# Performance work log

Measured on AMD Instinct MI355X. Metric: run time of the kernel, lower is better.

## Reference

```python
import jax, jax.numpy as jnp
import numpy as np

N_USERS = 50000
N_ENT = 100000
N_EDGES = 2_000_000
N_INTER = 1_000_000
CHANNEL = 64
N_HEADS = 2
D_K = CHANNEL // N_HEADS
N_HOPS = 2
N_REL = 10  # relation_emb has N_REL-1 rows


def setup_inputs() -> dict:
    key = jax.random.key(0)
    ks = jax.random.split(key, 8)
    user_emb = jax.random.normal(ks[0], (N_USERS, CHANNEL), jnp.float32) * 0.1
    entity_emb = jax.random.normal(ks[1], (N_ENT, CHANNEL), jnp.float32) * 0.1
    relation_emb = jax.random.normal(ks[2], (N_REL - 1, CHANNEL), jnp.float32) * 0.1
    W_Q = jax.random.normal(ks[3], (CHANNEL, CHANNEL), jnp.float32) * (1.0 / np.sqrt(CHANNEL))
    edge_index = jax.random.randint(ks[4], (2, N_EDGES), 0, N_ENT)
    edge_type = jax.random.randint(ks[5], (N_EDGES,), 1, N_REL)  # in [1, N_REL-1]
    inter_edge = jnp.stack([
        jax.random.randint(ks[6], (N_INTER,), 0, N_USERS),
        jax.random.randint(ks[7], (N_INTER,), 0, N_ENT),
    ])
    inter_edge_w = jnp.full((N_INTER,), 1.0 / 20.0, jnp.float32)
    return {
        "user_emb": user_emb,
        "entity_emb": entity_emb,
        "relation_emb": relation_emb,
        "W_Q": W_Q,
        "inter_edge_w": inter_edge_w,
        "edge_index": edge_index,
        "edge_type": edge_type,
        "inter_edge": inter_edge,
    }


def _l2norm(x):
    # F.normalize(dim=-1) with eps=1e-12
    n = jnp.linalg.norm(x, axis=-1, keepdims=True)
    return x / jnp.maximum(n, 1e-12)


def _scatter_softmax(logits, seg, num_segments):
    # per-segment (over leading axis) numerically-stable softmax; logits [E, H]
    m = jax.ops.segment_max(logits, seg, num_segments=num_segments)
    e = jnp.exp(logits - m[seg])
    s = jax.ops.segment_sum(e, seg, num_segments=num_segments)
    return e / s[seg]


def reference(user_emb, entity_emb, relation_emb, W_Q, inter_edge_w,
              edge_index, edge_type, inter_edge):
    head, tail = edge_index[0], edge_index[1]
    u_idx, i_idx = inter_edge[0], inter_edge[1]
    rel = relation_emb[edge_type - 1]  # [E, C]
    inv_sqrt_dk = 1.0 / np.sqrt(D_K)

    entity_res, user_res = entity_emb, user_emb
    for _ in range(N_HOPS):
        h_emb = entity_emb[head]                       # [E, C]
        t_emb = entity_emb[tail]                       # [E, C]
        q = (h_emb @ W_Q).reshape(-1, N_HEADS, D_K)    # [E, H, Dk]
        k = (t_emb @ W_Q).reshape(-1, N_HEADS, D_K) * rel.reshape(-1, N_HEADS, D_K)
        score = (q * k).sum(-1) * inv_sqrt_dk          # [E, H]
        attn = _scatter_softmax(score, head, N_ENT)    # [E, H]
        value = (t_emb * rel).reshape(-1, N_HEADS, D_K)
        agg = (value * attn[..., None]).reshape(-1, CHANNEL)
        entity_agg = jax.ops.segment_sum(agg, head, num_segments=N_ENT)
        item_agg = inter_edge_w[:, None] * entity_emb[i_idx]
        user_agg = jax.ops.segment_sum(item_agg, u_idx, num_segments=N_USERS)
        # mess_dropout disabled (eval mode)
        entity_emb = _l2norm(entity_agg)
        user_emb = _l2norm(user_agg)
        entity_res = entity_res + entity_emb
        user_res = user_res + user_emb
    return entity_res, user_res
```

## Files before the change

### kernel.cpp

```cpp
#include <hip/hip_runtime.h>

#define NU     50000
#define NEN    100000
#define NEDGE  2000000
#define NINTER 1000000
#define CH     64
#define NRELM1 9
#define CAPE   64
#define CAPU   64

#define BINSH   8
#define NBINE   ((NEN + 255) >> BINSH)
#define NBINU   ((NU  + 255) >> BINSH)
#define CHUNKE  8192
#define CHUNKU  4096
#define NBE_BLK ((NEDGE  + CHUNKE - 1) / CHUNKE)
#define NBU_BLK ((NINTER + CHUNKU - 1) / CHUNKU)
#define DSTRE   416
#define DSTRU   224
#define NSTR_E  ((NEN * CH) / 2048)
#define NSTR_U  ((NU * CH + 2047) / 2048)

typedef _Float16 hv2 __attribute__((ext_vector_type(2)));
typedef _Float16 h8  __attribute__((ext_vector_type(8)));
typedef float    f32x4 __attribute__((ext_vector_type(4)));
union P4 { float4 f; hv2 h[4]; };

static __device__ __forceinline__ hv2 pkrtz(float a, float b) {
    return __builtin_bit_cast(hv2, __builtin_amdgcn_cvt_pkrtz(a, b));
}


__global__ __launch_bounds__(256) void k_bin(
    const float* __restrict__ ue, const float* __restrict__ ee,
    const float* __restrict__ re, const float* __restrict__ wq,
    const float* __restrict__ iw, const int* __restrict__ eidx,
    const int* __restrict__ etype, const int* __restrict__ ii,
    _Float16* __restrict__ QE, float* __restrict__ Eres, float* __restrict__ Ures,
    _Float16* __restrict__ Relh, _Float16* __restrict__ Wt,
    unsigned* __restrict__ dirE, unsigned* __restrict__ dirU,
    int* __restrict__ blkBufE, unsigned long long* __restrict__ blkBufU)
{
    __shared__ long long srt64[CHUNKU];
    __shared__ int hist[512];
    __shared__ int sc[512];
    int* srt = (int*)srt64;
    int b = blockIdx.x, tid = threadIdx.x;

    if (b < NBE_BLK) {
        hist[tid] = 0; hist[tid + 256] = 0;
        __syncthreads();
        int base = b * CHUNKE;
        int n = NEDGE - base; if (n > CHUNKE) n = CHUNKE;
        for (int i = tid; i < n; i += 256)
            atomicAdd(&hist[eidx[base + i] >> BINSH], 1);
        __syncthreads();
        sc[tid] = hist[tid]; sc[tid + 256] = hist[tid + 256];
        __syncthreads();
#pragma unroll
        for (int off = 1; off < 512; off <<= 1) {
            int v0 = (tid >= off) ? sc[tid - off] : 0;
            int v1 = sc[tid + 256 - off];
            __syncthreads();
            sc[tid] += v0; sc[tid + 256] += v1;
            __syncthreads();
        }
        sc[tid] -= hist[tid]; sc[tid + 256] -= hist[tid + 256];
        __syncthreads();
        for (int i = tid; i < n; i += 256) {
            int h  = eidx[base + i];
            int t  = eidx[NEDGE + base + i];
            int rt = etype[base + i] - 1;
            int pos = atomicAdd(&sc[h >> BINSH], 1);
            srt[pos] = (h & 255) | ((t | (rt << 17)) << 8);
        }
        __syncthreads();
        int4* dst = (int4*)(blkBufE + b * CHUNKE);
        const int4* s4 = (const int4*)srt;
        for (int j = tid; j < ((n + 3) >> 2); j += 256) dst[j] = s4[j];
        for (int bin = tid; bin < NBINE; bin += 256)
            dirE[b * DSTRE + bin] =
                ((unsigned)(sc[bin] - hist[bin]) << 16) | (unsigned)hist[bin];
    } else if (b < NBE_BLK + NBU_BLK) {
        hist[tid] = 0; hist[tid + 256] = 0;
        __syncthreads();
        int ub = b - NBE_BLK;
        int base = ub * CHUNKU;
        int n = NINTER - base; if (n > CHUNKU) n = CHUNKU;
        for (int i = tid; i < n; i += 256)
            atomicAdd(&hist[ii[base + i] >> BINSH], 1);
        __syncthreads();
        sc[tid] = hist[tid]; sc[tid + 256] = hist[tid + 256];
        __syncthreads();
#pragma unroll
        for (int off = 1; off < 512; off <<= 1) {
            int v0 = (tid >= off) ? sc[tid - off] : 0;
            int v1 = sc[tid + 256 - off];
            __syncthreads();
            sc[tid] += v0; sc[tid + 256] += v1;
            __syncthreads();
        }
        sc[tid] -= hist[tid]; sc[tid + 256] -= hist[tid + 256];
        __syncthreads();
        for (int i = tid; i < n; i += 256) {
            int u = ii[base + i];
            int e = ii[NINTER + base + i];
            unsigned w = __float_as_uint(iw[base + i]);
            int pos = atomicAdd(&sc[u >> BINSH], 1);
            srt64[pos] = (unsigned long long)((u & 255) | (e << 8))
                       | ((unsigned long long)w << 32);
        }
        __syncthreads();
        int4* dst = (int4*)(blkBufU + (size_t)ub * CHUNKU);
        const int4* s4 = (const int4*)srt64;
        for (int j = tid; j < ((n + 1) >> 1); j += 256) dst[j] = s4[j];
        for (int bin = tid; bin < NBINU; bin += 256)
            dirU[ub * DSTRU + bin] =
                ((unsigned)(sc[bin] - hist[bin]) << 16) | (unsigned)hist[bin];
    } else {
        int sb = b - (NBE_BLK + NBU_BLK);
        if (sb < NSTR_E) {
            int i0 = sb * 2048 + tid * 8;
            float4 a = *(const float4*)(ee + i0);
            float4 c = *(const float4*)(ee + i0 + 4);
            *(float4*)(Eres + i0)     = a;
            *(float4*)(Eres + i0 + 4) = c;
            P4 o;
            o.h[0] = pkrtz(a.x, a.y);
            o.h[1] = pkrtz(a.z, a.w);
            o.h[2] = pkrtz(c.x, c.y);
            o.h[3] = pkrtz(c.z, c.w);
            int node = i0 >> 6, c0 = i0 & 63;
            *(float4*)(QE + (size_t)node * 128 + c0) = o.f;
        } else if (sb < NSTR_E + NSTR_U) {
            int i0 = (sb - NSTR_E) * 2048 + tid * 8;
            if (i0 < NU * CH) {
                *(float4*)(Ures + i0)     = *(const float4*)(ue + i0);
                *(float4*)(Ures + i0 + 4) = *(const float4*)(ue + i0 + 4);
            }
        } else {
            for (int i = tid; i < NRELM1 * CH; i += 256)
                Relh[i] = (_Float16)re[i];
            for (int i = tid; i < CH * CH; i += 256)
                Wt[(i & 63) * 64 + (i >> 6)] = (_Float16)wq[i];
        }
    }
}

__global__ __launch_bounds__(256) void k_place(
    const unsigned* __restrict__ dirE, const int* __restrict__ blkBufE,
    const unsigned* __restrict__ dirU, const unsigned long long* __restrict__ blkBufU,
    int* __restrict__ cntE, int* __restrict__ csrE,
    int* __restrict__ cntU, unsigned long long* __restrict__ csrU2)
{
    __shared__ int cnt[256];
    int b = blockIdx.x, tid = threadIdx.x;
    cnt[tid] = 0;
    __syncthreads();
    if (b < NBINE) {
        if (tid < NBE_BLK) {
            unsigned d = dirE[tid * DSTRE + b];
            int off = d >> 16, c = d & 0xFFFF;
            const int* src = blkBufE + tid * CHUNKE + off;
            for (int i = 0; i < c; ++i) {
                int rec = src[i];
                int nl = rec & 255;
                int pos = atomicAdd(&cnt[nl], 1);
                if (pos < CAPE) csrE[((b << BINSH) + nl) * CAPE + pos] = rec >> 8;
            }
        }
        __syncthreads();
        int node = (b << BINSH) + tid;
        if (node < NEN) { int c = cnt[tid]; cntE[node] = c > CAPE ? CAPE : c; }
    } else {
        int ub = b - NBINE;
        if (tid < NBU_BLK) {
            unsigned d = dirU[tid * DSTRU + ub];
            int off = d >> 16, c = d & 0xFFFF;
            const unsigned long long* src = blkBufU + (size_t)tid * CHUNKU + off;
            for (int i = 0; i < c; ++i) {
                unsigned long long rec = src[i];
                int nl = (int)rec & 255;
                int pos = atomicAdd(&cnt[nl], 1);
                if (pos < CAPU)
                    csrU2[((ub << BINSH) + nl) * CAPU + pos] =
                        ((rec & 0xFFFFFFFFull) >> 8) | (rec & 0xFFFFFFFF00000000ull);
            }
        }
        __syncthreads();
        int node = (ub << BINSH) + tid;
        if (node < NU) { int c = cnt[tid]; cntU[node] = c > CAPU ? CAPU : c; }
    }
}

__global__ __launch_bounds__(256) void k_gemm(
    _Float16* __restrict__ QE, const _Float16* __restrict__ Wt)
{
    int w = threadIdx.x >> 6, lane = threadIdx.x & 63;
    int r0 = blockIdx.x * 64 + w * 16;
    if (r0 >= NEN) return;
    int lr = lane & 15, lg = lane >> 4;
    const _Float16* arow = QE + (size_t)(r0 + lr) * 128 + lg * 8;
    h8 a0 = *(const h8*)(arow);
    h8 a1 = *(const h8*)(arow + 32);
#pragma unroll
    for (int ct = 0; ct < 4; ++ct) {
        const _Float16* brow = Wt + (ct * 16 + lr) * 64 + lg * 8;
        h8 b0 = *(const h8*)(brow);
        h8 b1 = *(const h8*)(brow + 32);
        f32x4 c = {0.f, 0.f, 0.f, 0.f};
        c = __builtin_amdgcn_mfma_f32_16x16x32_f16(a0, b0, c, 0, 0, 0);
        c = __builtin_amdgcn_mfma_f32_16x16x32_f16(a1, b1, c, 0, 0, 0);
#pragma unroll
        for (int r = 0; r < 4; ++r)
            QE[(size_t)(r0 + lg * 4 + r) * 128 + 64 + ct * 16 + lr] = (_Float16)c[r];
    }
}

__global__ __launch_bounds__(256) void k_fused(
    const int* __restrict__ cntE, const int* __restrict__ csrE,
    const _Float16* __restrict__ QE, const _Float16* __restrict__ Relh,
    _Float16* __restrict__ QEn, float* __restrict__ Eres,
    const int* __restrict__ cntU, const unsigned long long* __restrict__ csrU2,
    float* __restrict__ Ures)
{
    __shared__ __attribute__((aligned(16))) _Float16 RelL[NRELM1 * 64];
    int tid = threadIdx.x;
    if (tid < 72) *(float4*)(RelL + tid * 8) = *(const float4*)(Relh + tid * 8);
    __syncthreads();

    int wid  = blockIdx.x * 4 + (tid >> 6);
    int lane = tid & 63;
    int s = lane >> 3, l = lane & 7;
    int c8 = l * 8;

    if (wid < NEN) {
        int row = wid;
        int cnt = cntE[row];
        int beg = row * CAPE, end = beg + cnt;
        P4 q; q.f = *(const float4*)(QE + (size_t)row * 128 + 64 + c8);
        float acc[8] = {0.f,0.f,0.f,0.f,0.f,0.f,0.f,0.f};
        float den = 0.f;

        auto compute = [&](const P4& te, const P4& kt, const P4& rl, bool act) {
            float sc = 0.f;
#pragma unroll
            for (int i = 0; i < 4; ++i) {
                hv2 km = kt.h[i] * rl.h[i];
                sc = __builtin_amdgcn_fdot2(q.h[i], km, sc, false);
            }
            sc += __shfl_xor(sc, 1);
            sc += __shfl_xor(sc, 2);
            float ex = exp2f(sc * 0.25503489f);
            if (!act) ex = 0.f;
            den += ex;
#pragma unroll
            for (int i = 0; i < 4; ++i) {
                hv2 vm = te.h[i] * rl.h[i];
                acc[2*i]   += ex * (float)vm.x;
                acc[2*i+1] += ex * (float)vm.y;
            }
        };

        int p0 = beg + s;
        int iA = (p0 < end) ? csrE[p0] : 0;
        int iB = (p0 + 8 < end) ? csrE[p0 + 8] : 0;
        P4 teA, ktA, rlA;
        {
            const _Float16* bA = QE + (size_t)(iA & 0x1FFFF) * 128 + c8;
            teA.f = *(const float4*)bA;
            ktA.f = *(const float4*)(bA + 64);
            rlA.f = *(const float4*)(RelL + (iA >> 17) * 64 + c8);
        }
        for (int p = p0; p < end; p += 16) {
            P4 teB, ktB, rlB;
            {
                const _Float16* bB = QE + (size_t)(iB & 0x1FFFF) * 128 + c8;
                teB.f = *(const float4*)bB;
                ktB.f = *(const float4*)(bB + 64);
                rlB.f = *(const float4*)(RelL + (iB >> 17) * 64 + c8);
            }
            int iC = (p + 16 < end) ? csrE[p + 16] : 0;
            compute(teA, ktA, rlA, true);
            {
                const _Float16* bC = QE + (size_t)(iC & 0x1FFFF) * 128 + c8;
                teA.f = *(const float4*)bC;
                ktA.f = *(const float4*)(bC + 64);
                rlA.f = *(const float4*)(RelL + (iC >> 17) * 64 + c8);
            }
            int iD = (p + 24 < end) ? csrE[p + 24] : 0;
            compute(teB, ktB, rlB, p + 8 < end);
            iB = iD;
        }
        hv2 pk[4];
#pragma unroll
        for (int i = 0; i < 4; ++i)
            pk[i] = pkrtz(acc[2*i], acc[2*i+1]);
#pragma unroll
        for (int m = 8; m <= 32; m <<= 1) {
#pragma unroll
            for (int i = 0; i < 4; ++i) {
                int v = __shfl_xor(__builtin_bit_cast(int, pk[i]), m);
                pk[i] += __builtin_bit_cast(hv2, v);
            }
            den += __shfl_xor(den, m);
        }
        float af[8];
#pragma unroll
        for (int i = 0; i < 4; ++i) { af[2*i] = (float)pk[i].x; af[2*i+1] = (float)pk[i].y; }
        float invd = (den > 0.f) ? 1.f / den : 0.f;
        float ss = 0.f;
#pragma unroll
        for (int k = 0; k < 8; ++k) { af[k] *= invd; ss += af[k] * af[k]; }
        ss += __shfl_xor(ss, 1); ss += __shfl_xor(ss, 2); ss += __shfl_xor(ss, 4);
        float inv = 1.f / fmaxf(sqrtf(ss), 1e-12f);
#pragma unroll
        for (int k = 0; k < 8; ++k) af[k] *= inv;
        if (s == 0) {
            P4 o;
#pragma unroll
            for (int i = 0; i < 4; ++i)
                o.h[i] = pkrtz(af[2*i], af[2*i+1]);
            *(float4*)(QEn + (size_t)row * 128 + c8) = o.f;
            float4 r0 = *(const float4*)(Eres + (size_t)row * 64 + c8);
            float4 r1 = *(const float4*)(Eres + (size_t)row * 64 + c8 + 4);
            r0.x += af[0]; r0.y += af[1]; r0.z += af[2]; r0.w += af[3];
            r1.x += af[4]; r1.y += af[5]; r1.z += af[6]; r1.w += af[7];
            *(float4*)(Eres + (size_t)row * 64 + c8)     = r0;
            *(float4*)(Eres + (size_t)row * 64 + c8 + 4) = r1;
        }
    } else {
        int row = wid - NEN;
        int cnt = cntU[row];
        int beg = row * CAPU, end = beg + cnt;
        float acc[8] = {0.f,0.f,0.f,0.f,0.f,0.f,0.f,0.f};
        int p0 = beg + s;
        unsigned long long recA = (p0 < end) ? csrU2[p0] : 0ull;
        unsigned long long recB = (p0 + 8 < end) ? csrU2[p0 + 8] : 0ull;
        P4 teA; teA.f = *(const float4*)(QE + (size_t)(unsigned)recA * 128 + c8);
        for (int p = p0; p < end; p += 16) {
            P4 teB; teB.f = *(const float4*)(QE + (size_t)(unsigned)recB * 128 + c8);
            unsigned long long recC = (p + 16 < end) ? csrU2[p + 16] : 0ull;
            float wA = __uint_as_float((unsigned)(recA >> 32));
#pragma unroll
            for (int i = 0; i < 4; ++i) {
                acc[2*i]   += wA * (float)teA.h[i].x;
                acc[2*i+1] += wA * (float)teA.h[i].y;
            }
            teA.f = *(const float4*)(QE + (size_t)(unsigned)recC * 128 + c8);
            unsigned long long recD = (p + 24 < end) ? csrU2[p + 24] : 0ull;
            float wB = __uint_as_float((unsigned)(recB >> 32));
#pragma unroll
            for (int i = 0; i < 4; ++i) {
                acc[2*i]   += wB * (float)teB.h[i].x;
                acc[2*i+1] += wB * (float)teB.h[i].y;
            }
            recA = recC; recB = recD;
        }
        hv2 pk[4];
#pragma unroll
        for (int i = 0; i < 4; ++i)
            pk[i] = pkrtz(acc[2*i], acc[2*i+1]);
#pragma unroll
        for (int m = 8; m <= 32; m <<= 1) {
#pragma unroll
            for (int i = 0; i < 4; ++i) {
                int v = __shfl_xor(__builtin_bit_cast(int, pk[i]), m);
                pk[i] += __builtin_bit_cast(hv2, v);
            }
        }
        float af[8];
#pragma unroll
        for (int i = 0; i < 4; ++i) { af[2*i] = (float)pk[i].x; af[2*i+1] = (float)pk[i].y; }
        float ss = 0.f;
#pragma unroll
        for (int k = 0; k < 8; ++k) ss += af[k] * af[k];
        ss += __shfl_xor(ss, 1); ss += __shfl_xor(ss, 2); ss += __shfl_xor(ss, 4);
        float inv = 1.f / fmaxf(sqrtf(ss), 1e-12f);
        if (s == 0) {
            float4 r0 = *(const float4*)(Ures + (size_t)row * 64 + c8);
            float4 r1 = *(const float4*)(Ures + (size_t)row * 64 + c8 + 4);
            r0.x += af[0] * inv; r0.y += af[1] * inv; r0.z += af[2] * inv; r0.w += af[3] * inv;
            r1.x += af[4] * inv; r1.y += af[5] * inv; r1.z += af[6] * inv; r1.w += af[7] * inv;
            *(float4*)(Ures + (size_t)row * 64 + c8)     = r0;
            *(float4*)(Ures + (size_t)row * 64 + c8 + 4) = r1;
        }
    }
}

extern "C" void kernel_launch(void* const* d_in, const int* in_sizes, int n_in,
                              void* d_out, int out_size, void* d_ws, size_t ws_size,
                              hipStream_t stream)
{
    const float* ue = (const float*)d_in[0];
    const float* ee = (const float*)d_in[1];
    const float* re = (const float*)d_in[2];
    const float* wq = (const float*)d_in[3];
    const float* iw = (const float*)d_in[4];
    const int* eidx  = (const int*)d_in[5];
    const int* etype = (const int*)d_in[6];
    const int* ii    = (const int*)d_in[7];

    float* Eres = (float*)d_out;
    float* Ures = Eres + (size_t)NEN * CH;

    _Float16* Relh = (_Float16*)d_ws;
    _Float16* Wt   = Relh + 1024;
    _Float16* QEA  = Wt + 4096;
    _Float16* QEB  = QEA + (size_t)NEN * 128;
    int* cntE      = (int*)(QEB + (size_t)NEN * 128);
    int* cntU      = cntE + NEN;
    int* csrE      = cntU + NU;
    unsigned long long* csrU2 = (unsigned long long*)(csrE + (size_t)NEN * CAPE);
    unsigned* dirE = (unsigned*)(csrU2 + (size_t)NU * CAPU);
    unsigned* dirU = dirE + NBE_BLK * DSTRE;
    int* blkBufE   = (int*)QEB;
    unsigned long long* blkBufU =
        (unsigned long long*)((char*)QEB + (size_t)NBE_BLK * CHUNKE * 4);

    k_bin<<<NBE_BLK + NBU_BLK + NSTR_E + NSTR_U + 1, 256, 0, stream>>>(
        ue, ee, re, wq, iw, eidx, etype, ii,
        QEA, Eres, Ures, Relh, Wt, dirE, dirU, blkBufE, blkBufU);
    k_place<<<NBINE + NBINU, 256, 0, stream>>>(dirE, blkBufE, dirU, blkBufU,
                                               cntE, csrE, cntU, csrU2);

    _Float16* QEc = QEA;
    _Float16* QEn = QEB;
    for (int hop = 0; hop < 2; ++hop) {
        k_gemm <<<(NEN + 63) / 64, 256, 0, stream>>>(QEc, Wt);
        k_fused<<<(NEN + NU) / 4, 256, 0, stream>>>(cntE, csrE, QEc, Relh,
                                                    QEn, Eres, cntU, csrU2, Ures);
        _Float16* tmp = QEc; QEc = QEn; QEn = tmp;
    }
}
```

Measured before the change: 448.2 us.

## Process two rows per wavefront using half-wave groups in fused aggregation kernel

Each 64-lane wavefront now handles two destination rows (entity or user), one per 32-lane half, with 4 edge slots per row instead of 8. This halves the grid and is meant to cut lane idling on rows with few edges (average degree about 20). The edge loop becomes a rolling one-ahead prefetch with a single compute step per iteration, the cross-slot reductions drop one shuffle stage, and the shared relation table is padded to a 72-element row stride to spread LDS banks. Each lane now walks twice as many serial iterations per row, which may expose more gather latency.

```diff
diff --git a/kernel.cpp b/kernel.cpp
--- a/kernel.cpp
+++ b/kernel.cpp
@@ -224,14 +224,16 @@
     const int* __restrict__ cntU, const unsigned long long* __restrict__ csrU2,
     float* __restrict__ Ures)
 {
-    __shared__ __attribute__((aligned(16))) _Float16 RelL[NRELM1 * 64];
+    __shared__ __attribute__((aligned(16))) _Float16 RelL[NRELM1 * 72];
     int tid = threadIdx.x;
-    if (tid < 72) *(float4*)(RelL + tid * 8) = *(const float4*)(Relh + tid * 8);
+    if (tid < 72) *(float4*)(RelL + (tid >> 3) * 72 + (tid & 7) * 8)
+                      = *(const float4*)(Relh + tid * 8);
     __syncthreads();
 
-    int wid  = blockIdx.x * 4 + (tid >> 6);
+    int pair = blockIdx.x * 4 + (tid >> 6);
     int lane = tid & 63;
-    int s = lane >> 3, l = lane & 7;
+    int wid  = pair * 2 + (lane >> 5);
+    int s = (lane >> 3) & 3, l = lane & 7;
     int c8 = l * 8;
 
     if (wid < NEN) {
@@ -242,11 +244,32 @@
         float acc[8] = {0.f,0.f,0.f,0.f,0.f,0.f,0.f,0.f};
         float den = 0.f;
 
-        auto compute = [&](const P4& te, const P4& kt, const P4& rl, bool act) {
+        int a0 = beg + s;
+        int iA = (a0 < end) ? csrE[a0] : 0;
+        int iB = (a0 + 4 < end) ? csrE[a0 + 4] : 0;
+        P4 teA, ktA, rlA;
+        {
+            const _Float16* bA = QE + (size_t)(iA & 0x1FFFF) * 128 + c8;
+            teA.f = *(const float4*)bA;
+            ktA.f = *(const float4*)(bA + 64);
+            rlA.f = *(const float4*)(RelL + (iA >> 17) * 72 + c8);
+        }
+        int nit = (cnt + 3) >> 2;
+        for (int it = 0; it < nit; ++it) {
+            P4 teB, ktB, rlB;
+            {
+                const _Float16* bB = QE + (size_t)(iB & 0x1FFFF) * 128 + c8;
+                teB.f = *(const float4*)bB;
+                ktB.f = *(const float4*)(bB + 64);
+                rlB.f = *(const float4*)(RelL + (iB >> 17) * 72 + c8);
+            }
+            int a2 = a0 + (it + 2) * 4;
+            int iN = (a2 < end) ? csrE[a2] : 0;
+            bool act = (a0 + it * 4) < end;
             float sc = 0.f;
 #pragma unroll
             for (int i = 0; i < 4; ++i) {
-                hv2 km = kt.h[i] * rl.h[i];
+                hv2 km = ktA.h[i] * rlA.h[i];
                 sc = __builtin_amdgcn_fdot2(q.h[i], km, sc, false);
             }
             sc += __shfl_xor(sc, 1);
@@ -256,48 +279,18 @@
             den += ex;
 #pragma unroll
             for (int i = 0; i < 4; ++i) {
-                hv2 vm = te.h[i] * rl.h[i];
+                hv2 vm = teA.h[i] * rlA.h[i];
                 acc[2*i]   += ex * (float)vm.x;
                 acc[2*i+1] += ex * (float)vm.y;
             }
-        };
-
-        int p0 = beg + s;
-        int iA = (p0 < end) ? csrE[p0] : 0;
-        int iB = (p0 + 8 < end) ? csrE[p0 + 8] : 0;
-        P4 teA, ktA, rlA;
-        {
-            const _Float16* bA = QE + (size_t)(iA & 0x1FFFF) * 128 + c8;
-            teA.f = *(const float4*)bA;
-            ktA.f = *(const float4*)(bA + 64);
-            rlA.f = *(const float4*)(RelL + (iA >> 17) * 64 + c8);
-        }
-        for (int p = p0; p < end; p += 16) {
-            P4 teB, ktB, rlB;
-            {
-                const _Float16* bB = QE + (size_t)(iB & 0x1FFFF) * 128 + c8;
-                teB.f = *(const float4*)bB;
-                ktB.f = *(const float4*)(bB + 64);
-                rlB.f = *(const float4*)(RelL + (iB >> 17) * 64 + c8);
-            }
-            int iC = (p + 16 < end) ? csrE[p + 16] : 0;
-            compute(teA, ktA, rlA, true);
-            {
-                const _Float16* bC = QE + (size_t)(iC & 0x1FFFF) * 128 + c8;
-                teA.f = *(const float4*)bC;
-                ktA.f = *(const float4*)(bC + 64);
-                rlA.f = *(const float4*)(RelL + (iC >> 17) * 64 + c8);
-            }
-            int iD = (p + 24 < end) ? csrE[p + 24] : 0;
-            compute(teB, ktB, rlB, p + 8 < end);
-            iB = iD;
+            teA = teB; ktA = ktB; rlA = rlB; iB = iN;
         }
         hv2 pk[4];
 #pragma unroll
         for (int i = 0; i < 4; ++i)
             pk[i] = pkrtz(acc[2*i], acc[2*i+1]);
 #pragma unroll
-        for (int m = 8; m <= 32; m <<= 1) {
+        for (int m = 8; m <= 16; m <<= 1) {
 #pragma unroll
             for (int i = 0; i < 4; ++i) {
                 int v = __shfl_xor(__builtin_bit_cast(int, pk[i]), m);
@@ -334,35 +327,29 @@
         int cnt = cntU[row];
         int beg = row * CAPU, end = beg + cnt;
         float acc[8] = {0.f,0.f,0.f,0.f,0.f,0.f,0.f,0.f};
-        int p0 = beg + s;
-        unsigned long long recA = (p0 < end) ? csrU2[p0] : 0ull;
-        unsigned long long recB = (p0 + 8 < end) ? csrU2[p0 + 8] : 0ull;
+        int a0 = beg + s;
+        unsigned long long recA = (a0 < end) ? csrU2[a0] : 0ull;
+        unsigned long long recB = (a0 + 4 < end) ? csrU2[a0 + 4] : 0ull;
         P4 teA; teA.f = *(const float4*)(QE + (size_t)(unsigned)recA * 128 + c8);
-        for (int p = p0; p < end; p += 16) {
+        int nit = (cnt + 3) >> 2;
+        for (int it = 0; it < nit; ++it) {
             P4 teB; teB.f = *(const float4*)(QE + (size_t)(unsigned)recB * 128 + c8);
-            unsigned long long recC = (p + 16 < end) ? csrU2[p + 16] : 0ull;
+            int a2 = a0 + (it + 2) * 4;
+            unsigned long long recN = (a2 < end) ? csrU2[a2] : 0ull;
             float wA = __uint_as_float((unsigned)(recA >> 32));
 #pragma unroll
             for (int i = 0; i < 4; ++i) {
                 acc[2*i]   += wA * (float)teA.h[i].x;
                 acc[2*i+1] += wA * (float)teA.h[i].y;
             }
-            teA.f = *(const float4*)(QE + (size_t)(unsigned)recC * 128 + c8);
-            unsigned long long recD = (p + 24 < end) ? csrU2[p + 24] : 0ull;
-            float wB = __uint_as_float((unsigned)(recB >> 32));
-#pragma unroll
-            for (int i = 0; i < 4; ++i) {
-                acc[2*i]   += wB * (float)teB.h[i].x;
-                acc[2*i+1] += wB * (float)teB.h[i].y;
-            }
-            recA = recC; recB = recD;
+            teA = teB; recA = recB; recB = recN;
         }
         hv2 pk[4];
 #pragma unroll
         for (int i = 0; i < 4; ++i)
             pk[i] = pkrtz(acc[2*i], acc[2*i+1]);
 #pragma unroll
-        for (int m = 8; m <= 32; m <<= 1) {
+        for (int m = 8; m <= 16; m <<= 1) {
 #pragma unroll
             for (int i = 0; i < 4; ++i) {
                 int v = __shfl_xor(__builtin_bit_cast(int, pk[i]), m);
@@ -428,7 +415,7 @@
     _Float16* QEn = QEB;
     for (int hop = 0; hop < 2; ++hop) {
         k_gemm <<<(NEN + 63) / 64, 256, 0, stream>>>(QEc, Wt);
-        k_fused<<<(NEN + NU) / 4, 256, 0, stream>>>(cntE, csrE, QEc, Relh,
+        k_fused<<<(NEN + NU) / 8, 256, 0, stream>>>(cntE, csrE, QEc, Relh,
                                                     QEn, Eres, cntU, csrU2, Ures);
         _Float16* tmp = QEc; QEc = QEn; QEn = tmp;
     }
```

New measurement: 418.3 us. 6.7% less time.
